# Performance work log

Measured on AMD Instinct MI355X. Metric: run time of the kernel, lower is better.

## Reference

```python
import jax, jax.numpy as jnp
import numpy as np

EPS = 1e-5


def _conv_w(x, k):
    # cross-correlation along width, kernel size 2, padding 1 -> width W+1
    xp = jnp.pad(x, ((0, 0), (0, 0), (0, 0), (1, 1)))
    return k[0] * xp[..., :-1] + k[1] * xp[..., 1:]


def _conv_h(x, k):
    # cross-correlation along height, kernel size 2, padding 1 -> height H+1
    xp = jnp.pad(x, ((0, 0), (0, 0), (1, 1), (0, 0)))
    return k[0] * xp[..., :-1, :] + k[1] * xp[..., 1:, :]


def _dwt(x, lp, hp):
    L = _conv_h(_conv_w(x, lp), lp)
    Hc = _conv_h(_conv_w(x, hp), hp)
    return L[:, :, ::2, ::2], Hc[:, :, ::2, ::2]


def _bn(y, g, b, m, v):
    # eval-mode batchnorm over channel axis 1
    scale = (g / jnp.sqrt(v + EPS))[None, :, None, None]
    shift = (b - m * g / jnp.sqrt(v + EPS))[None, :, None, None]
    return y * scale + shift


def setup_inputs() -> dict:
    key = jax.random.key(0)
    ks = jax.random.split(key, 8)
    S, B, H, W, C = 5, 8, 512, 512, 64
    x = jax.random.normal(ks[0], (B, 1, H, W), dtype=jnp.float32)
    lp = jnp.tile(jnp.array([0.7071, 0.7071], dtype=jnp.float32), (S, 1))
    hp = jnp.tile(jnp.array([0.7071, -0.7071], dtype=jnp.float32), (S, 1))
    w1 = jax.random.normal(ks[1], (S, C, 1), dtype=jnp.float32) * 0.5
    w2 = jax.random.normal(ks[2], (S, C, C), dtype=jnp.float32) * (1.0 / np.sqrt(C))
    g1 = jnp.ones((S, C), jnp.float32)
    b1 = jnp.zeros((S, C), jnp.float32)
    m1 = jax.random.normal(ks[3], (S, C), dtype=jnp.float32) * 0.1
    v1 = jax.random.uniform(ks[4], (S, C), dtype=jnp.float32) + 0.5
    g2 = jnp.ones((S, C), jnp.float32)
    b2 = jnp.zeros((S, C), jnp.float32)
    m2 = jax.random.normal(ks[5], (S, C), dtype=jnp.float32) * 0.1
    v2 = jax.random.uniform(ks[6], (S, C), dtype=jnp.float32) + 0.5
    return dict(x=x, lp=lp, hp=hp, w1=w1, w2=w2, g1=g1, b1=b1, m1=m1, v1=v1,
                g2=g2, b2=b2, m2=m2, v2=v2)


def reference(x, lp, hp, w1, w2, g1, b1, m1, v1, g2, b2, m2, v2):
    # Returns stacked-over-scale (L, H_coeff, processed_L):
    #   L, Hc: [S, B, 1, H', W'];  P: [S, B, 64, H', W']
    def per_scale(lp_s, hp_s, w1_s, g1_s, b1_s, m1_s, v1_s,
                  w2_s, g2_s, b2_s, m2_s, v2_s):
        L, Hc = _dwt(x, lp_s, hp_s)
        y = jnp.einsum('oc,bchw->bohw', w1_s, L)
        y = jax.nn.relu(_bn(y, g1_s, b1_s, m1_s, v1_s))
        y = jnp.einsum('oc,bchw->bohw', w2_s, y)
        y = jax.nn.relu(_bn(y, g2_s, b2_s, m2_s, v2_s))
        return L, Hc, y

    return jax.vmap(per_scale)(lp, hp, w1, g1, b1, m1, v1, w2, g2, b2, m2, v2)
```

## Files before the change

### kernel.cpp

```cpp
#include <hip/hip_runtime.h>
#include <math.h>

#define EPSF 1e-5f

constexpr int Sn = 5, Bn = 8, Hin = 512, Win = 512, Cn = 64;
constexpr int HO = 257, WO = 257;
constexpr int HW = HO * WO;
constexpr int NPIX = Bn * HW;
constexpr int TOTPIX = Sn * NPIX;

constexpr int WSF = 64 + Cn * 66 * 2;

__global__ __launch_bounds__(64) void precompute_kernel(
    const float* __restrict__ w1, const float* __restrict__ w2,
    const float* __restrict__ g1, const float* __restrict__ b1,
    const float* __restrict__ m1, const float* __restrict__ v1,
    const float* __restrict__ g2, const float* __restrict__ b2,
    const float* __restrict__ m2, const float* __restrict__ v2,
    float* __restrict__ ws) {
    int s = blockIdx.x;
    int c = threadIdx.x;
    __shared__ float sa1[Cn], st1[Cn], stc[Cn], stS[Cn];
    __shared__ int   scS[Cn];

    int idx = s * Cn + c;
    float sc1 = g1[idx] / sqrtf(v1[idx] + EPSF);
    float a1  = sc1 * w1[idx];
    float t1  = b1[idx] - m1[idx] * sc1;
    sa1[c] = a1;
    st1[c] = t1;
    float tc = (a1 != 0.f) ? (-t1 / a1) : INFINITY;
    stc[c] = tc;
    __syncthreads();

    int rk = 0;
    for (int c2 = 0; c2 < Cn; c2++) {
        float t = stc[c2];
        rk += (t < tc) || (t == tc && c2 < c);
    }
    stS[rk] = tc;
    scS[rk] = c;
    __syncthreads();

    float* wss = ws + (size_t)s * WSF;
    wss[c] = stS[c];

    int o = c;
    float sc2 = g2[idx] / sqrtf(v2[idx] + EPSF);
    float t2o = b2[idx] - m2[idx] * sc2;
    const float* w2row = w2 + ((size_t)s * Cn + o) * Cn;

    float alpha = 0.f, beta = t2o;
    for (int cc = 0; cc < Cn; cc++) {
        float a = sa1[cc];
        bool act = (a < 0.f) || (a == 0.f && st1[cc] > 0.f);
        if (act) {
            float wf = sc2 * w2row[cc];
            alpha = fmaf(wf, a, alpha);
            beta  = fmaf(wf, st1[cc], beta);
        }
    }
    float2* abrow = (float2*)(wss + Cn);
    abrow[o * 66 + 0] = make_float2(alpha, beta);

    for (int r = 1; r <= Cn; r++) {
        int cc = scS[r - 1];
        float a = sa1[cc];
        if (a != 0.f) {
            float wf = sc2 * w2row[cc];
            float sgn = (a > 0.f) ? 1.f : -1.f;
            alpha = fmaf(sgn * wf, a, alpha);
            beta  = fmaf(sgn * wf, st1[cc], beta);
        }
        abrow[o * 66 + r] = make_float2(alpha, beta);
    }
}

constexpr int GPT = 4;
constexpr int TPB = 256;
constexpr int PIXPB = TPB * GPT;
constexpr int NCHUNK = (HW + PIXPB - 1) / PIXPB;

__device__ __forceinline__ float pwl(const float2 ab, float v) {
    return fmaxf(fmaf(ab.x, v, ab.y), 0.f);
}

__global__ __launch_bounds__(TPB) void fused_kernel(
    const float* __restrict__ x,
    const float* __restrict__ lp, const float* __restrict__ hp,
    const float* __restrict__ ws,
    float* __restrict__ Lout, float* __restrict__ Hout,
    float* __restrict__ Pout) {
    __shared__ float  stS[Cn];
    __shared__ float2 sab[Cn * 66];

    const int tid = threadIdx.x;
    const int b = blockIdx.y, s = blockIdx.z;
    const float* wss = ws + (size_t)s * WSF;
    if (tid < Cn) stS[tid] = wss[tid];
    const float2* abg = (const float2*)(wss + Cn);
    for (int t = tid; t < Cn * 66; t += TPB) sab[t] = abg[t];
    __syncthreads();

    const int pbase = (blockIdx.x * TPB + tid) * GPT;
    if (pbase >= HW) return;

    const float l0 = lp[2 * s], l1 = lp[2 * s + 1];
    const float h0 = hp[2 * s], h1 = hp[2 * s + 1];
    const float* xb = x + (size_t)b * (Hin * Win);

    float Lv[GPT + 3];
    float Hv[GPT];
    int   lo7[GPT + 3];

    #pragma unroll
    for (int q = 0; q < GPT + 3; ++q) {
        const int px = pbase + q;
        float Lq = 0.f, Hq = 0.f;
        if (px < HW) {
            const int i = px / WO;
            const int j = px - i * WO;
            const int r0 = 2 * i - 1, r1 = 2 * i;
            const int c0 = 2 * j - 1, c1 = 2 * j;
            const float x00 = (r0 >= 0  && c0 >= 0 ) ? xb[r0 * Win + c0] : 0.f;
            const float x01 = (r0 >= 0  && c1 < Win) ? xb[r0 * Win + c1] : 0.f;
            const float x10 = (r1 < Hin && c0 >= 0 ) ? xb[r1 * Win + c0] : 0.f;
            const float x11 = (r1 < Hin && c1 < Win) ? xb[r1 * Win + c1] : 0.f;
            Lq = l0 * (l0 * x00 + l1 * x01) + l1 * (l0 * x10 + l1 * x11);
            Hq = h0 * (h0 * x00 + h1 * x01) + h1 * (h0 * x10 + h1 * x11);
        }
        Lv[q] = Lq;
        if (q < GPT) Hv[q] = Hq;
        int lo = 0, hi = Cn;
        while (lo < hi) {
            const int mid = (lo + hi) >> 1;
            if (stS[mid] < Lq) lo = mid + 1; else hi = mid;
        }
        lo7[q] = lo;
    }

    {
        const size_t lbase = (size_t)(s * Bn + b) * HW + pbase;
        #pragma unroll
        for (int q = 0; q < GPT; ++q) {
            if (pbase + q < HW) {
                Lout[lbase + q] = Lv[q];
                Hout[lbase + q] = Hv[q];
            }
        }
    }

    float* const Pb = Pout + ((size_t)(s * Bn + b) * Cn) * HW + pbase;

    if (pbase + GPT + 3 <= HW) {
        float* po = Pb;
        #pragma unroll 2
        for (int o = 0; o < Cn; o += 4, po += (size_t)4 * HW) {
            {
                const float2 a0 = sab[o * 66 + lo7[0]];
                const float2 a1 = sab[o * 66 + lo7[1]];
                const float2 a2 = sab[o * 66 + lo7[2]];
                const float2 a3 = sab[o * 66 + lo7[3]];
                const float4 v = make_float4(pwl(a0, Lv[0]), pwl(a1, Lv[1]),
                                             pwl(a2, Lv[2]), pwl(a3, Lv[3]));
                *(float4*)(po) = v;
            }
            {
                const float2 a0 = sab[(o + 1) * 66 + lo7[3]];
                const float2 a1 = sab[(o + 1) * 66 + lo7[4]];
                const float2 a2 = sab[(o + 1) * 66 + lo7[5]];
                const float2 a3 = sab[(o + 1) * 66 + lo7[6]];
                const float4 v = make_float4(pwl(a0, Lv[3]), pwl(a1, Lv[4]),
                                             pwl(a2, Lv[5]), pwl(a3, Lv[6]));
                *(float4*)(po + HW + 3) = v;
            }
            {
                const float2 a0 = sab[(o + 2) * 66 + lo7[2]];
                const float2 a1 = sab[(o + 2) * 66 + lo7[3]];
                const float2 a2 = sab[(o + 2) * 66 + lo7[4]];
                const float2 a3 = sab[(o + 2) * 66 + lo7[5]];
                const float4 v = make_float4(pwl(a0, Lv[2]), pwl(a1, Lv[3]),
                                             pwl(a2, Lv[4]), pwl(a3, Lv[5]));
                *(float4*)(po + 2 * (size_t)HW + 2) = v;
            }
            {
                const float2 a0 = sab[(o + 3) * 66 + lo7[1]];
                const float2 a1 = sab[(o + 3) * 66 + lo7[2]];
                const float2 a2 = sab[(o + 3) * 66 + lo7[3]];
                const float2 a3 = sab[(o + 3) * 66 + lo7[4]];
                const float4 v = make_float4(pwl(a0, Lv[1]), pwl(a1, Lv[2]),
                                             pwl(a2, Lv[3]), pwl(a3, Lv[4]));
                *(float4*)(po + 3 * (size_t)HW + 1) = v;
            }
        }
        if (pbase == 0) {
            float* ph = Pb;
            for (int o = 0; o < Cn; ++o, ph += HW) {
                const int d = (4 - (o & 3)) & 3;
                if (d > 0) ph[0] = pwl(sab[o * 66 + lo7[0]], Lv[0]);
                if (d > 1) ph[1] = pwl(sab[o * 66 + lo7[1]], Lv[1]);
                if (d > 2) ph[2] = pwl(sab[o * 66 + lo7[2]], Lv[2]);
            }
        }
    } else {
        #pragma unroll
        for (int q = 0; q < GPT; ++q) {
            const int px = pbase + q;
            if (px >= HW) break;
            const float Lq = Lv[q];
            const int   r  = lo7[q];
            float* Pp = Pb + q;
            #pragma unroll 8
            for (int o = 0; o < Cn; ++o) {
                Pp[(size_t)o * HW] = pwl(sab[o * 66 + r], Lq);
            }
        }
    }
}

extern "C" void kernel_launch(void* const* d_in, const int* in_sizes, int n_in,
                              void* d_out, int out_size, void* d_ws, size_t ws_size,
                              hipStream_t stream) {
    const float* x  = (const float*)d_in[0];
    const float* lp = (const float*)d_in[1];
    const float* hp = (const float*)d_in[2];
    const float* w1 = (const float*)d_in[3];
    const float* w2 = (const float*)d_in[4];
    const float* g1 = (const float*)d_in[5];
    const float* b1 = (const float*)d_in[6];
    const float* m1 = (const float*)d_in[7];
    const float* v1 = (const float*)d_in[8];
    const float* g2 = (const float*)d_in[9];
    const float* b2 = (const float*)d_in[10];
    const float* m2 = (const float*)d_in[11];
    const float* v2 = (const float*)d_in[12];

    float* out  = (float*)d_out;
    float* Lout = out;
    float* Hout = out + TOTPIX;
    float* Pout = out + 2 * TOTPIX;
    float* ws   = (float*)d_ws;

    precompute_kernel<<<Sn, Cn, 0, stream>>>(w1, w2, g1, b1, m1, v1,
                                             g2, b2, m2, v2, ws);

    dim3 grid(NCHUNK, Bn, Sn);
    fused_kernel<<<grid, TPB, 0, stream>>>(x, lp, hp, ws, Lout, Hout, Pout);
}
```

Baseline: 789.3 us.

## Share halo pixels via wave shuffles, vectorize L/H stores, use nontemporal stores

Each thread now computes only its own 4 DWT pixels and gets the 3 halo pixels from the next lane through shuffles. Only the last lane of each wave recomputes its halo. The L and H outputs are written as aligned float4 nontemporal stores, using a per-slice alignment offset. The large P output also moves to nontemporal vector stores, and launch bounds now request 4 blocks per SM. The goal is to cut redundant loads and binary searches, and to stop the huge streaming output from polluting the cache. In exchange, lane 63's extra work causes divergence, and the early return for out-of-range threads is gone.

```diff
diff --git a/kernel.cpp b/kernel.cpp
--- a/kernel.cpp
+++ b/kernel.cpp
@@ -10,6 +10,8 @@
 constexpr int TOTPIX = Sn * NPIX;
 
 constexpr int WSF = 64 + Cn * 66 * 2;
+
+typedef float f32x4 __attribute__((ext_vector_type(4)));
 
 __global__ __launch_bounds__(64) void precompute_kernel(
     const float* __restrict__ w1, const float* __restrict__ w2,
@@ -85,7 +87,28 @@
     return fmaxf(fmaf(ab.x, v, ab.y), 0.f);
 }
 
-__global__ __launch_bounds__(TPB) void fused_kernel(
+__device__ __forceinline__ void dwt_one(
+    const float* __restrict__ xb, int i, int j,
+    float l0, float l1, float h0, float h1,
+    const float* __restrict__ stS_,
+    float& Lq, float& Hq, int& lo_out) {
+    const int r0 = 2 * i - 1, r1 = 2 * i;
+    const int c0 = 2 * j - 1, c1 = 2 * j;
+    const float x00 = (r0 >= 0 && r0 < Hin && c0 >= 0 ) ? xb[r0 * Win + c0] : 0.f;
+    const float x01 = (r0 >= 0 && r0 < Hin && c1 < Win) ? xb[r0 * Win + c1] : 0.f;
+    const float x10 = (r1 < Hin && c0 >= 0 )            ? xb[r1 * Win + c0] : 0.f;
+    const float x11 = (r1 < Hin && c1 < Win)            ? xb[r1 * Win + c1] : 0.f;
+    Lq = l0 * (l0 * x00 + l1 * x01) + l1 * (l0 * x10 + l1 * x11);
+    Hq = h0 * (h0 * x00 + h1 * x01) + h1 * (h0 * x10 + h1 * x11);
+    int lo = 0, hi = Cn;
+    while (lo < hi) {
+        const int mid = (lo + hi) >> 1;
+        if (stS_[mid] < Lq) lo = mid + 1; else hi = mid;
+    }
+    lo_out = lo;
+}
+
+__global__ __launch_bounds__(TPB, 4) void fused_kernel(
     const float* __restrict__ x,
     const float* __restrict__ lp, const float* __restrict__ hp,
     const float* __restrict__ ws,
@@ -102,95 +125,107 @@
     for (int t = tid; t < Cn * 66; t += TPB) sab[t] = abg[t];
     __syncthreads();
 
-    const int pbase = (blockIdx.x * TPB + tid) * GPT;
-    if (pbase >= HW) return;
-
     const float l0 = lp[2 * s], l1 = lp[2 * s + 1];
     const float h0 = hp[2 * s], h1 = hp[2 * s + 1];
     const float* xb = x + (size_t)b * (Hin * Win);
 
+    const int pbase = (blockIdx.x * TPB + tid) * GPT;
+
     float Lv[GPT + 3];
-    float Hv[GPT];
+    float Hv[GPT + 3];
     int   lo7[GPT + 3];
 
+    int i = pbase / WO;
+    int j = pbase - i * WO;
     #pragma unroll
-    for (int q = 0; q < GPT + 3; ++q) {
-        const int px = pbase + q;
-        float Lq = 0.f, Hq = 0.f;
-        if (px < HW) {
-            const int i = px / WO;
-            const int j = px - i * WO;
-            const int r0 = 2 * i - 1, r1 = 2 * i;
-            const int c0 = 2 * j - 1, c1 = 2 * j;
-            const float x00 = (r0 >= 0  && c0 >= 0 ) ? xb[r0 * Win + c0] : 0.f;
-            const float x01 = (r0 >= 0  && c1 < Win) ? xb[r0 * Win + c1] : 0.f;
-            const float x10 = (r1 < Hin && c0 >= 0 ) ? xb[r1 * Win + c0] : 0.f;
-            const float x11 = (r1 < Hin && c1 < Win) ? xb[r1 * Win + c1] : 0.f;
-            Lq = l0 * (l0 * x00 + l1 * x01) + l1 * (l0 * x10 + l1 * x11);
-            Hq = h0 * (h0 * x00 + h1 * x01) + h1 * (h0 * x10 + h1 * x11);
-        }
-        Lv[q] = Lq;
-        if (q < GPT) Hv[q] = Hq;
-        int lo = 0, hi = Cn;
-        while (lo < hi) {
-            const int mid = (lo + hi) >> 1;
-            if (stS[mid] < Lq) lo = mid + 1; else hi = mid;
-        }
-        lo7[q] = lo;
-    }
+    for (int q = 0; q < GPT; ++q) {
+        dwt_one(xb, i, j, l0, l1, h0, h1, stS, Lv[q], Hv[q], lo7[q]);
+        if (++j == WO) { j = 0; ++i; }
+    }
+    Lv[4] = __shfl_down(Lv[0], 1, 64);  Hv[4] = __shfl_down(Hv[0], 1, 64);
+    lo7[4] = __shfl_down(lo7[0], 1, 64);
+    Lv[5] = __shfl_down(Lv[1], 1, 64);  Hv[5] = __shfl_down(Hv[1], 1, 64);
+    lo7[5] = __shfl_down(lo7[1], 1, 64);
+    Lv[6] = __shfl_down(Lv[2], 1, 64);  Hv[6] = __shfl_down(Hv[2], 1, 64);
+    lo7[6] = __shfl_down(lo7[2], 1, 64);
+    if ((tid & 63) == 63) {
+        #pragma unroll
+        for (int q = GPT; q < GPT + 3; ++q) {
+            dwt_one(xb, i, j, l0, l1, h0, h1, stS, Lv[q], Hv[q], lo7[q]);
+            if (++j == WO) { j = 0; ++i; }
+        }
+    }
+
+    const int sb = s * Bn + b;
+    const bool fast = (pbase + GPT + 3 <= HW);
 
     {
-        const size_t lbase = (size_t)(s * Bn + b) * HW + pbase;
-        #pragma unroll
-        for (int q = 0; q < GPT; ++q) {
-            if (pbase + q < HW) {
-                Lout[lbase + q] = Lv[q];
-                Hout[lbase + q] = Hv[q];
-            }
-        }
-    }
-
-    float* const Pb = Pout + ((size_t)(s * Bn + b) * Cn) * HW + pbase;
-
-    if (pbase + GPT + 3 <= HW) {
+        const size_t lb = (size_t)sb * HW + pbase;
+        const int dlt = (4 - (sb & 3)) & 3;
+        if (fast) {
+            f32x4 l4, h4;
+            switch (dlt) {
+                case 0:  l4 = f32x4{Lv[0], Lv[1], Lv[2], Lv[3]};
+                         h4 = f32x4{Hv[0], Hv[1], Hv[2], Hv[3]}; break;
+                case 1:  l4 = f32x4{Lv[1], Lv[2], Lv[3], Lv[4]};
+                         h4 = f32x4{Hv[1], Hv[2], Hv[3], Hv[4]}; break;
+                case 2:  l4 = f32x4{Lv[2], Lv[3], Lv[4], Lv[5]};
+                         h4 = f32x4{Hv[2], Hv[3], Hv[4], Hv[5]}; break;
+                default: l4 = f32x4{Lv[3], Lv[4], Lv[5], Lv[6]};
+                         h4 = f32x4{Hv[3], Hv[4], Hv[5], Hv[6]}; break;
+            }
+            __builtin_nontemporal_store(l4, (f32x4*)(Lout + lb + dlt));
+            __builtin_nontemporal_store(h4, (f32x4*)(Hout + lb + dlt));
+            if (pbase == 0) {
+                if (dlt > 0) { Lout[lb + 0] = Lv[0]; Hout[lb + 0] = Hv[0]; }
+                if (dlt > 1) { Lout[lb + 1] = Lv[1]; Hout[lb + 1] = Hv[1]; }
+                if (dlt > 2) { Lout[lb + 2] = Lv[2]; Hout[lb + 2] = Hv[2]; }
+            }
+        } else {
+            #pragma unroll
+            for (int q = 0; q < GPT; ++q) {
+                if (pbase + q < HW) {
+                    Lout[lb + q] = Lv[q];
+                    Hout[lb + q] = Hv[q];
+                }
+            }
+        }
+    }
+
+    float* const Pb = Pout + ((size_t)sb * Cn) * HW + pbase;
+
+    if (fast) {
         float* po = Pb;
         #pragma unroll 2
-        for (int o = 0; o < Cn; o += 4, po += (size_t)4 * HW) {
-            {
-                const float2 a0 = sab[o * 66 + lo7[0]];
-                const float2 a1 = sab[o * 66 + lo7[1]];
-                const float2 a2 = sab[o * 66 + lo7[2]];
-                const float2 a3 = sab[o * 66 + lo7[3]];
-                const float4 v = make_float4(pwl(a0, Lv[0]), pwl(a1, Lv[1]),
-                                             pwl(a2, Lv[2]), pwl(a3, Lv[3]));
-                *(float4*)(po) = v;
-            }
-            {
-                const float2 a0 = sab[(o + 1) * 66 + lo7[3]];
-                const float2 a1 = sab[(o + 1) * 66 + lo7[4]];
-                const float2 a2 = sab[(o + 1) * 66 + lo7[5]];
-                const float2 a3 = sab[(o + 1) * 66 + lo7[6]];
-                const float4 v = make_float4(pwl(a0, Lv[3]), pwl(a1, Lv[4]),
-                                             pwl(a2, Lv[5]), pwl(a3, Lv[6]));
-                *(float4*)(po + HW + 3) = v;
-            }
-            {
-                const float2 a0 = sab[(o + 2) * 66 + lo7[2]];
-                const float2 a1 = sab[(o + 2) * 66 + lo7[3]];
-                const float2 a2 = sab[(o + 2) * 66 + lo7[4]];
-                const float2 a3 = sab[(o + 2) * 66 + lo7[5]];
-                const float4 v = make_float4(pwl(a0, Lv[2]), pwl(a1, Lv[3]),
-                                             pwl(a2, Lv[4]), pwl(a3, Lv[5]));
-                *(float4*)(po + 2 * (size_t)HW + 2) = v;
-            }
-            {
-                const float2 a0 = sab[(o + 3) * 66 + lo7[1]];
-                const float2 a1 = sab[(o + 3) * 66 + lo7[2]];
-                const float2 a2 = sab[(o + 3) * 66 + lo7[3]];
-                const float2 a3 = sab[(o + 3) * 66 + lo7[4]];
-                const float4 v = make_float4(pwl(a0, Lv[1]), pwl(a1, Lv[2]),
-                                             pwl(a2, Lv[3]), pwl(a3, Lv[4]));
-                *(float4*)(po + 3 * (size_t)HW + 1) = v;
+        for (int og = 0; og < Cn / 4; ++og, po += (size_t)4 * HW) {
+            const int o = og * 4;
+            {
+                f32x4 v = f32x4{pwl(sab[o * 66 + lo7[0]], Lv[0]),
+                                pwl(sab[o * 66 + lo7[1]], Lv[1]),
+                                pwl(sab[o * 66 + lo7[2]], Lv[2]),
+                                pwl(sab[o * 66 + lo7[3]], Lv[3])};
+                __builtin_nontemporal_store(v, (f32x4*)po);
+            }
+            {
+                f32x4 v = f32x4{pwl(sab[(o + 1) * 66 + lo7[3]], Lv[3]),
+                                pwl(sab[(o + 1) * 66 + lo7[4]], Lv[4]),
+                                pwl(sab[(o + 1) * 66 + lo7[5]], Lv[5]),
+                                pwl(sab[(o + 1) * 66 + lo7[6]], Lv[6])};
+                __builtin_nontemporal_store(v, (f32x4*)(po + HW + 3));
+            }
+            {
+                f32x4 v = f32x4{pwl(sab[(o + 2) * 66 + lo7[2]], Lv[2]),
+                                pwl(sab[(o + 2) * 66 + lo7[3]], Lv[3]),
+                                pwl(sab[(o + 2) * 66 + lo7[4]], Lv[4]),
+                                pwl(sab[(o + 2) * 66 + lo7[5]], Lv[5])};
+                __builtin_nontemporal_store(v, (f32x4*)(po + 2 * (size_t)HW + 2));
+            }
+            {
+                f32x4 v = f32x4{pwl(sab[(o + 3) * 66 + lo7[1]], Lv[1]),
+                                pwl(sab[(o + 3) * 66 + lo7[2]], Lv[2]),
+                                pwl(sab[(o + 3) * 66 + lo7[3]], Lv[3]),
+                                pwl(sab[(o + 3) * 66 + lo7[4]], Lv[4])};
+                __builtin_nontemporal_store(v, (f32x4*)(po + 3 * (size_t)HW + 1));
             }
         }
         if (pbase == 0) {
@@ -230,6 +265,7 @@
     const float* b1 = (const float*)d_in[6];
     const float* m1 = (const float*)d_in[7];
     const float* v1 = (const float*)d_in[8];
+    const float* m2_unused = nullptr; (void)m2_unused;
     const float* g2 = (const float*)d_in[9];
     const float* b2 = (const float*)d_in[10];
     const float* m2 = (const float*)d_in[11];
```

Result: no change. 798.8 us (+1.2%).
